# Optimization experiments

Measured on AMD Instinct MI355X. Metric: run time of the kernel, lower is better.

## Reference

```python
import jax, jax.numpy as jnp
import numpy as np

IN_F, OUT_F, GROUP = 4096, 11008, 128
TOKENS = 64


def setup_inputs() -> dict:
    key = jax.random.key(0)
    k1, k2, k3, k4 = jax.random.split(key, 4)
    x = jax.random.normal(k1, (TOKENS, IN_F), dtype=jnp.float32).astype(jnp.float16)
    # packed uint8 values stored in int32 (two int4 nibbles per byte)
    w_packed = jax.random.randint(k2, (IN_F, OUT_F // 2), 0, 256, dtype=jnp.int32)
    num_groups = IN_F // GROUP
    w_scale = (jax.random.uniform(k3, (num_groups, OUT_F), minval=1e-3, maxval=0.1)).astype(jnp.float16)
    w_zero = jnp.round(jax.random.uniform(k4, (num_groups, OUT_F), minval=0.0, maxval=15.0)).astype(jnp.float16)
    return {"x": x, "w_packed": w_packed, "w_scale": w_scale, "w_zero": w_zero}


def _dequantize_int4(w_packed, w_scale, w_zero, group_size=GROUP):
    in_f = w_packed.shape[0]
    out_f = w_packed.shape[1] * 2
    w_low = (w_packed & 15).astype(jnp.float16)          # even output columns
    w_high = ((w_packed >> 4) & 15).astype(jnp.float16)  # odd output columns
    # interleave low/high -> [in_f, out_f]
    w_int4 = jnp.stack([w_low, w_high], axis=-1).reshape(in_f, out_f)
    num_groups = in_f // group_size
    w_g = w_int4.reshape(num_groups, group_size, out_f)
    w = (w_g - w_zero[:, None, :]) * w_scale[:, None, :]
    return w.reshape(in_f, out_f)


def reference(x, w_packed, w_scale, w_zero):
    w = _dequantize_int4(w_packed, w_scale, w_zero)  # [in_f, out_f] fp16
    return jnp.matmul(x.astype(jnp.float16), w)      # [tokens, out_f]
```

## Files before the change

kernel.cpp:

```cpp
#include <hip/hip_runtime.h>
#include <stdint.h>

#define IN_F   4096
#define OUT_F  11008
#define C32    5504
#define LDST   72
#define KHALF  2048
#define NST    32

typedef __attribute__((ext_vector_type(8))) _Float16 half8;
typedef __attribute__((ext_vector_type(4))) float floatx4;

static __device__ __forceinline__ uint32_t pkh(float a, float b) {
    auto h = __builtin_amdgcn_cvt_pkrtz(a, b);
    union { decltype(h) v; uint32_t u; } r; r.v = h; return r.u;
}

__global__ __launch_bounds__(256) void prep_kernel(
    const float* __restrict__ x, uint32_t* __restrict__ xh, float4* __restrict__ out4)
{
    int tid = blockIdx.x * 256 + threadIdx.x;
    if (tid < (64 * OUT_F / 4)) out4[tid] = make_float4(0.f, 0.f, 0.f, 0.f);
    if (tid < (64 * IN_F / 2)) {
        float2 v = ((const float2*)x)[tid];
        xh[tid] = pkh(v.x, v.y);
    }
}

__global__ __launch_bounds__(256, 4) void int4_gemm_kernel(
    const int*      __restrict__ wp,
    const float*    __restrict__ wscale,
    const float*    __restrict__ wzero,
    const uint32_t* __restrict__ xh,
    float*          __restrict__ out)
{
    __shared__ float4 tab[16 * 16];
    __shared__ __align__(16) ushort bld[2][32 * LDST];

    const int tid   = threadIdx.x;
    const int col0  = blockIdx.x * 32;
    const int ky    = blockIdx.y;
    const int kbase = ky * KHALF;

    const int c  = tid & 15;
    const int kb = (tid >> 4) * 4;
    const int ce = 2 * c, co = ce + 1;
    const int* wbase = wp + (size_t)(kbase + kb) * C32 + (col0 >> 1) + c;

    const int wave = tid >> 6;
    const int lane = tid & 63;
    const int g    = lane >> 4;
    const int bc0  = lane & 15;
    const int bc1  = bc0 + 16;
    const uint32_t* xbase = xh + (size_t)(wave * 16 + bc0) * (IN_F / 2) + (kbase >> 1) + g * 4;

    {
        int gg = tid >> 4, cp = tid & 15;
        size_t b = (size_t)(ky * 16 + gg) * OUT_F + col0 + 2 * cp;
        float se = wscale[b], so = wscale[b + 1];
        float ze = wzero[b],  zo = wzero[b + 1];
        tab[tid] = make_float4(se, ze * se, so, zo * so);
    }

    floatx4 acc0 = {0.f, 0.f, 0.f, 0.f}, acc1 = {0.f, 0.f, 0.f, 0.f};

    struct Pref { uint32_t q0, q1, q2, q3; };
    auto issue = [&](int st) {
        const int* p = wbase + (size_t)st * (64 * (size_t)C32);
        Pref P;
        P.q0 = (uint32_t)p[0];
        P.q1 = (uint32_t)p[C32];
        P.q2 = (uint32_t)p[2 * C32];
        P.q3 = (uint32_t)p[3 * C32];
        return P;
    };

    auto dq_write = [&](ushort* buf, const Pref& P, int st) {
        float4 t = tab[((st >> 1) << 4) + c];
        float l0 = fmaf((float)( P.q0        & 15u), t.x, -t.y);
        float l1 = fmaf((float)( P.q1        & 15u), t.x, -t.y);
        float l2 = fmaf((float)( P.q2        & 15u), t.x, -t.y);
        float l3 = fmaf((float)( P.q3        & 15u), t.x, -t.y);
        float h0 = fmaf((float)((P.q0 >> 4)  & 15u), t.z, -t.w);
        float h1 = fmaf((float)((P.q1 >> 4)  & 15u), t.z, -t.w);
        float h2 = fmaf((float)((P.q2 >> 4)  & 15u), t.z, -t.w);
        float h3 = fmaf((float)((P.q3 >> 4)  & 15u), t.z, -t.w);
        *(uint2*)(buf + ce * LDST + kb) = make_uint2(pkh(l0, l1), pkh(l2, l3));
        *(uint2*)(buf + co * LDST + kb) = make_uint2(pkh(h0, h1), pkh(h2, h3));
    };

    auto compute = [&](const ushort* buf, int st) {
        union { uint4 u; half8 h; } a0, a1;
        a0.u = *(const uint4*)(xbase + (size_t)st * 32);
        a1.u = *(const uint4*)(xbase + (size_t)st * 32 + 16);
        half8 B00 = *(const half8*)(buf + bc0 * LDST + g * 8);
        half8 B01 = *(const half8*)(buf + bc0 * LDST + 32 + g * 8);
        half8 B10 = *(const half8*)(buf + bc1 * LDST + g * 8);
        half8 B11 = *(const half8*)(buf + bc1 * LDST + 32 + g * 8);
        acc0 = __builtin_amdgcn_mfma_f32_16x16x32_f16(a0.h, B00, acc0, 0, 0, 0);
        acc1 = __builtin_amdgcn_mfma_f32_16x16x32_f16(a0.h, B10, acc1, 0, 0, 0);
        acc0 = __builtin_amdgcn_mfma_f32_16x16x32_f16(a1.h, B01, acc0, 0, 0, 0);
        acc1 = __builtin_amdgcn_mfma_f32_16x16x32_f16(a1.h, B11, acc1, 0, 0, 0);
    };

    Pref P = issue(0);
    __syncthreads();
    dq_write(bld[0], P, 0);
    P = issue(1);
    asm volatile("s_waitcnt lgkmcnt(0)");
    __builtin_amdgcn_s_barrier();

    #pragma unroll 2
    for (int st = 0; st < NST; ++st) {
        if (st + 1 < NST) {
            Pref Pn = (st + 2 < NST) ? issue(st + 2) : P;
            dq_write(bld[(st + 1) & 1], P, st + 1);
            P = Pn;
        }
        compute(bld[st & 1], st);
        asm volatile("s_waitcnt lgkmcnt(0)");
        __builtin_amdgcn_s_barrier();
    }

    const int ocol = col0 + bc0;
    const int rb   = wave * 16 + g * 4;
    #pragma unroll
    for (int r = 0; r < 4; ++r) {
        unsafeAtomicAdd(out + (size_t)(rb + r) * OUT_F + ocol,      acc0[r]);
        unsafeAtomicAdd(out + (size_t)(rb + r) * OUT_F + ocol + 16, acc1[r]);
    }
}

extern "C" void kernel_launch(void* const* d_in, const int* in_sizes, int n_in,
                              void* d_out, int out_size, void* d_ws, size_t ws_size,
                              hipStream_t stream) {
    const float* x      = (const float*)d_in[0];
    const int*   wp     = (const int*)  d_in[1];
    const float* wscale = (const float*)d_in[2];
    const float* wzero  = (const float*)d_in[3];
    float*       out    = (float*)d_out;
    uint32_t*    xh     = (uint32_t*)d_ws;
    (void)in_sizes; (void)n_in; (void)out_size; (void)ws_size;

    prep_kernel<<<dim3(688), dim3(256), 0, stream>>>(x, xh, (float4*)out);
    int4_gemm_kernel<<<dim3(344, 2), dim3(256), 0, stream>>>(wp, wscale, wzero, xh, out);
}
```

Measured before the change: 41.44 us.

## Widen column tile to 128, split K eight ways, vectorize weight loads with swizzled LDS

```diff
diff --git a/kernel.cpp b/kernel.cpp
--- a/kernel.cpp
+++ b/kernel.cpp
@@ -4,9 +4,13 @@
 #define IN_F   4096
 #define OUT_F  11008
 #define C32    5504
-#define LDST   72
-#define KHALF  2048
-#define NST    32
+#define KSPL   8
+#define KBLK   512
+#define NST    8
+#define NGRPL  4
+#define COLS   128
+#define DCOLS  64
+#define LDSTR  144
 
 typedef __attribute__((ext_vector_type(8))) _Float16 half8;
 typedef __attribute__((ext_vector_type(4))) float floatx4;
@@ -34,100 +38,108 @@
     const uint32_t* __restrict__ xh,
     float*          __restrict__ out)
 {
-    __shared__ float4 tab[16 * 16];
-    __shared__ __align__(16) ushort bld[2][32 * LDST];
+    __shared__ float4 tab[NGRPL * 64];
+    __shared__ __align__(16) ushort bld[2][COLS * 72];
 
     const int tid   = threadIdx.x;
-    const int col0  = blockIdx.x * 32;
+    const int bx    = blockIdx.x;
     const int ky    = blockIdx.y;
-    const int kbase = ky * KHALF;
+    const int col0  = bx * COLS;
+    const int kbase = ky * KBLK;
 
-    const int c  = tid & 15;
-    const int kb = (tid >> 4) * 4;
-    const int ce = 2 * c, co = ce + 1;
-    const int* wbase = wp + (size_t)(kbase + kb) * C32 + (col0 >> 1) + c;
+    const int c4 = tid & 15;
+    const int kq = tid >> 4;
+    const int* wbase = wp + (size_t)(kbase + kq * 4) * C32 + bx * DCOLS + c4 * 4;
 
-    const int wave = tid >> 6;
-    const int lane = tid & 63;
-    const int g    = lane >> 4;
-    const int bc0  = lane & 15;
-    const int bc1  = bc0 + 16;
-    const uint32_t* xbase = xh + (size_t)(wave * 16 + bc0) * (IN_F / 2) + (kbase >> 1) + g * 4;
+    const int wv = tid >> 6;
+    const int g  = (tid & 63) >> 4;
+    const int bc = tid & 15;
+    const uint32_t* xA = xh + (size_t)(wv * 16 + bc) * (IN_F / 2) + (kbase >> 1) + g * 4;
 
     {
-        int gg = tid >> 4, cp = tid & 15;
-        size_t b = (size_t)(ky * 16 + gg) * OUT_F + col0 + 2 * cp;
+        int gg = tid >> 6, cp = tid & 63;
+        size_t b = (size_t)(ky * NGRPL + gg) * OUT_F + col0 + 2 * cp;
         float se = wscale[b], so = wscale[b + 1];
         float ze = wzero[b],  zo = wzero[b + 1];
-        tab[tid] = make_float4(se, ze * se, so, zo * so);
+        tab[gg * 64 + cp] = make_float4(se, ze * se, so, zo * so);
     }
 
-    floatx4 acc0 = {0.f, 0.f, 0.f, 0.f}, acc1 = {0.f, 0.f, 0.f, 0.f};
+    floatx4 acc[8];
+    #pragma unroll
+    for (int i = 0; i < 8; ++i) acc[i] = floatx4{0.f, 0.f, 0.f, 0.f};
 
-    struct Pref { uint32_t q0, q1, q2, q3; };
+    struct WSet { uint4 w[4]; };
     auto issue = [&](int st) {
-        const int* p = wbase + (size_t)st * (64 * (size_t)C32);
-        Pref P;
-        P.q0 = (uint32_t)p[0];
-        P.q1 = (uint32_t)p[C32];
-        P.q2 = (uint32_t)p[2 * C32];
-        P.q3 = (uint32_t)p[3 * C32];
-        return P;
+        const int* p = wbase + (size_t)(st * 64) * C32;
+        WSet S;
+        #pragma unroll
+        for (int j = 0; j < 4; ++j)
+            S.w[j] = *(const uint4*)(p + (size_t)j * C32);
+        return S;
     };
 
-    auto dq_write = [&](ushort* buf, const Pref& P, int st) {
-        float4 t = tab[((st >> 1) << 4) + c];
-        float l0 = fmaf((float)( P.q0        & 15u), t.x, -t.y);
-        float l1 = fmaf((float)( P.q1        & 15u), t.x, -t.y);
-        float l2 = fmaf((float)( P.q2        & 15u), t.x, -t.y);
-        float l3 = fmaf((float)( P.q3        & 15u), t.x, -t.y);
-        float h0 = fmaf((float)((P.q0 >> 4)  & 15u), t.z, -t.w);
-        float h1 = fmaf((float)((P.q1 >> 4)  & 15u), t.z, -t.w);
-        float h2 = fmaf((float)((P.q2 >> 4)  & 15u), t.z, -t.w);
-        float h3 = fmaf((float)((P.q3 >> 4)  & 15u), t.z, -t.w);
-        *(uint2*)(buf + ce * LDST + kb) = make_uint2(pkh(l0, l1), pkh(l2, l3));
-        *(uint2*)(buf + co * LDST + kb) = make_uint2(pkh(h0, h1), pkh(h2, h3));
+    const int wblk = (((kq >> 1) ^ (c4 & 7)) & 7) * 16 + (kq & 1) * 8;
+
+    auto dq_write = [&](ushort* buf, const WSet& S, int st) {
+        #pragma unroll
+        for (int d = 0; d < 4; ++d) {
+            float4 t = tab[(st >> 1) * 64 + 4 * c4 + d];
+            float e[4], o[4];
+            #pragma unroll
+            for (int j = 0; j < 4; ++j) {
+                uint32_t q = ((const uint32_t*)&S.w[j])[d];
+                e[j] = fmaf((float)( q       & 15u), t.x, -t.y);
+                o[j] = fmaf((float)((q >> 4) & 15u), t.z, -t.w);
+            }
+            const int ce = 8 * c4 + 2 * d;
+            *(uint2*)((char*)buf + ce * LDSTR       + wblk) = make_uint2(pkh(e[0], e[1]), pkh(e[2], e[3]));
+            *(uint2*)((char*)buf + (ce + 1) * LDSTR + wblk) = make_uint2(pkh(o[0], o[1]), pkh(o[2], o[3]));
+        }
     };
 
     auto compute = [&](const ushort* buf, int st) {
-        union { uint4 u; half8 h; } a0, a1;
-        a0.u = *(const uint4*)(xbase + (size_t)st * 32);
-        a1.u = *(const uint4*)(xbase + (size_t)st * 32 + 16);
-        half8 B00 = *(const half8*)(buf + bc0 * LDST + g * 8);
-        half8 B01 = *(const half8*)(buf + bc0 * LDST + 32 + g * 8);
-        half8 B10 = *(const half8*)(buf + bc1 * LDST + g * 8);
-        half8 B11 = *(const half8*)(buf + bc1 * LDST + 32 + g * 8);
-        acc0 = __builtin_amdgcn_mfma_f32_16x16x32_f16(a0.h, B00, acc0, 0, 0, 0);
-        acc1 = __builtin_amdgcn_mfma_f32_16x16x32_f16(a0.h, B10, acc1, 0, 0, 0);
-        acc0 = __builtin_amdgcn_mfma_f32_16x16x32_f16(a1.h, B01, acc0, 0, 0, 0);
-        acc1 = __builtin_amdgcn_mfma_f32_16x16x32_f16(a1.h, B11, acc1, 0, 0, 0);
+        union { uint4 u; half8 h; } A0, A1;
+        A0.u = *(const uint4*)(xA + st * 32);
+        A1.u = *(const uint4*)(xA + st * 32 + 16);
+        #pragma unroll
+        for (int sc = 0; sc < 8; ++sc) {
+            const int col = sc * 16 + bc;
+            const char* cb = (const char*)buf + col * LDSTR;
+            const int xr = (col >> 3) & 7;
+            half8 B0 = *(const half8*)(cb + (( g      ^ xr) & 7) * 16);
+            half8 B1 = *(const half8*)(cb + (((4 + g) ^ xr) & 7) * 16);
+            acc[sc] = __builtin_amdgcn_mfma_f32_16x16x32_f16(A0.h, B0, acc[sc], 0, 0, 0);
+            acc[sc] = __builtin_amdgcn_mfma_f32_16x16x32_f16(A1.h, B1, acc[sc], 0, 0, 0);
+        }
     };
 
-    Pref P = issue(0);
+    WSet Pa = issue(0);
+    WSet Pb = issue(1);
     __syncthreads();
-    dq_write(bld[0], P, 0);
-    P = issue(1);
+    dq_write(bld[0], Pa, 0);
+    Pa = issue(2);
     asm volatile("s_waitcnt lgkmcnt(0)");
     __builtin_amdgcn_s_barrier();
 
     #pragma unroll 2
     for (int st = 0; st < NST; ++st) {
         if (st + 1 < NST) {
-            Pref Pn = (st + 2 < NST) ? issue(st + 2) : P;
-            dq_write(bld[(st + 1) & 1], P, st + 1);
-            P = Pn;
+            if ((st & 1) == 0) { dq_write(bld[(st + 1) & 1], Pb, st + 1); if (st + 3 < NST) Pb = issue(st + 3); }
+            else               { dq_write(bld[(st + 1) & 1], Pa, st + 1); if (st + 3 < NST) Pa = issue(st + 3); }
         }
         compute(bld[st & 1], st);
         asm volatile("s_waitcnt lgkmcnt(0)");
         __builtin_amdgcn_s_barrier();
     }
 
-    const int ocol = col0 + bc0;
-    const int rb   = wave * 16 + g * 4;
+    const int ocol = col0 + bc;
+    const int orow = wv * 16 + g * 4;
     #pragma unroll
-    for (int r = 0; r < 4; ++r) {
-        unsafeAtomicAdd(out + (size_t)(rb + r) * OUT_F + ocol,      acc0[r]);
-        unsafeAtomicAdd(out + (size_t)(rb + r) * OUT_F + ocol + 16, acc1[r]);
+    for (int sc = 0; sc < 8; ++sc) {
+        #pragma unroll
+        for (int r = 0; r < 4; ++r) {
+            unsafeAtomicAdd(out + (size_t)(orow + r) * OUT_F + ocol + sc * 16, acc[sc][r]);
+        }
     }
 }
 
@@ -143,5 +155,5 @@
     (void)in_sizes; (void)n_in; (void)out_size; (void)ws_size;
 
     prep_kernel<<<dim3(688), dim3(256), 0, stream>>>(x, xh, (float4*)out);
-    int4_gemm_kernel<<<dim3(344, 2), dim3(256), 0, stream>>>(wp, wscale, wzero, xh, out);
+    int4_gemm_kernel<<<dim3(OUT_F / COLS, KSPL), dim3(256), 0, stream>>>(wp, wscale, wzero, xh, out);
 }
```

Measured after the change: 43.31 us. +4.5%, slower.
